# Kernel tuning notes

Measured on AMD Instinct MI355X. Metric: run time of the kernel, lower is better.

## Reference

```python
import jax, jax.numpy as jnp
import numpy as np

B = 1048576  # batch size
D = 16       # in_dim == hid_dim == out_dim (required by the torch matmul broadcasting)


def setup_inputs() -> dict:
    key = jax.random.key(0)
    kx, kw = jax.random.split(key)
    x = jax.random.normal(kx, (B, D), dtype=jnp.float32)
    W = jax.random.normal(kw, (D, D, D), dtype=jnp.float32) * (1.0 / D)
    return {"x": x, "W": W}


def reference(x, W):
    # Original torch: xBx = x @ W @ x.T permuted, then take the batch diagonal.
    # Mathematically: out[b, k] = sum_{i, j} x[b, i] * W[k, i, j] * x[b, j]
    # (batched bilinear/quadratic form per output channel k). We compute only
    # the needed diagonal terms instead of the full BxB cross-batch product.
    return jnp.einsum('bi,kij,bj->bk', x, W, x)
```

## Files before the change

### kernel.cpp

```cpp
#include <hip/hip_runtime.h>
#include <hip/hip_bf16.h>


typedef __attribute__((ext_vector_type(8)))  short  short8;
typedef __attribute__((ext_vector_type(8)))  __bf16 bf16x8;
typedef __attribute__((ext_vector_type(4)))  float  floatx4;

#define DEV static __device__ __forceinline__

constexpr int  alpha_of(int c) { return (c < 32) ? (c & 3) : (c - 32); }
constexpr int  beta_of(int c)  { return (c < 32) ? ((c & 3) + (c >> 2)) : (c - 32 + 8); }
constexpr bool live_of(int c)  { return c < 36; }

template <int C>
DEV float pval(const float* xv) {
    if constexpr (!live_of(C)) return 0.f;
    else return xv[alpha_of(C)] * xv[beta_of(C)];
}

template <int S>
DEV short8 make_afrag(const float* xv) {
    union { short8 s; __hip_bfloat162 h[4]; } u;
    u.h[0] = __float22bfloat162_rn(make_float2(pval<8 * S + 0>(xv), pval<8 * S + 1>(xv)));
    u.h[1] = __float22bfloat162_rn(make_float2(pval<8 * S + 2>(xv), pval<8 * S + 3>(xv)));
    u.h[2] = __float22bfloat162_rn(make_float2(pval<8 * S + 4>(xv), pval<8 * S + 5>(xv)));
    u.h[3] = __float22bfloat162_rn(make_float2(pval<8 * S + 6>(xv), pval<8 * S + 7>(xv)));
    return u.s;
}

DEV floatx4 mfma_bf16(short8 a, short8 b, floatx4 c) {
    return __builtin_amdgcn_mfma_f32_16x16x32_bf16(
        __builtin_bit_cast(bf16x8, a), __builtin_bit_cast(bf16x8, b), c, 0, 0, 0);
}

DEV float q_elem(const float* __restrict__ W, int e) {
    const int n = e / 160;
    const int k = e - n * 160;
    const int s = k >> 5, q = (k >> 3) & 3, j = k & 7;
    const int c = 8 * s + j;
    float qv = 0.f;
    if (c < 36) {
        const int a = (c < 32) ? (c & 3) : (c - 32);
        const int b = (c < 32) ? ((c & 3) + (c >> 2)) : (c - 32 + 8);
        const float w = (c < 32) ? 1.0f : 0.5f;
        const int I = (a + 4 * q) & 15, J = (b + 4 * q) & 15;
        qv = (I == J) ? W[n * 256 + I * 16 + I]
                      : w * (W[n * 256 + I * 16 + J] + W[n * 256 + J * 16 + I]);
    }
    return qv;
}

__global__ __launch_bounds__(256, 8)
void bilinear16_kernel(const float* __restrict__ x, const float* __restrict__ W,
                       float* __restrict__ out, int ntiles) {
    __shared__ __align__(16) short Qt[16][160];
    const int tid = threadIdx.x;
    for (int e = tid; e < 16 * 160; e += 256) {
        __hip_bfloat16 h = __float2bfloat16(q_elem(W, e));
        Qt[0][e] = *reinterpret_cast<short*>(&h);
    }
    __syncthreads();

    const int lane = tid & 63;
    const int n    = lane & 15;
    const int q    = lane >> 4;

    const short8 b0 = *reinterpret_cast<const short8*>(&Qt[n][0 * 32 + q * 8]);
    const short8 b1 = *reinterpret_cast<const short8*>(&Qt[n][1 * 32 + q * 8]);
    const short8 b2 = *reinterpret_cast<const short8*>(&Qt[n][2 * 32 + q * 8]);
    const short8 b3 = *reinterpret_cast<const short8*>(&Qt[n][3 * 32 + q * 8]);
    const short8 b4 = *reinterpret_cast<const short8*>(&Qt[n][4 * 32 + q * 8]);

    const int waveId = blockIdx.x * 4 + (tid >> 6);
    const int nwaves = gridDim.x * 4;

    for (int t = waveId; t < ntiles; t += nwaves) {
        const float4* xr = reinterpret_cast<const float4*>(x + (size_t)(t * 16 + n) * 16);
        const float4 c0 = xr[q];
        const float4 c1 = xr[(q + 1) & 3];
        const float4 c2 = xr[(q + 2) & 3];
        const float xv[12] = {c0.x, c0.y, c0.z, c0.w,
                              c1.x, c1.y, c1.z, c1.w,
                              c2.x, c2.y, c2.z, c2.w};

        floatx4 acc = {0.f, 0.f, 0.f, 0.f};
        acc = mfma_bf16(make_afrag<0>(xv), b0, acc);
        acc = mfma_bf16(make_afrag<1>(xv), b1, acc);
        acc = mfma_bf16(make_afrag<2>(xv), b2, acc);
        acc = mfma_bf16(make_afrag<3>(xv), b3, acc);
        acc = mfma_bf16(make_afrag<4>(xv), b4, acc);

        float* ob = out + (size_t)t * 256 + q * 64 + n;
        ob[0]  = acc[0];
        ob[16] = acc[1];
        ob[32] = acc[2];
        ob[48] = acc[3];
    }
}

extern "C" void kernel_launch(void* const* d_in, const int* in_sizes, int n_in,
                              void* d_out, int out_size, void* d_ws, size_t ws_size,
                              hipStream_t stream) {
    const float* x = (const float*)d_in[0];
    const float* W = (const float*)d_in[1];
    float* out = (float*)d_out;
    const int Bn = in_sizes[0] / 16;
    const int ntiles = Bn >> 4;
    bilinear16_kernel<<<2048, 256, 0, stream>>>(x, W, out, ntiles);
}
```

Before: 126.5 us.

## Load one float4 per lane with shuffles and stage outputs for coalesced stores

```diff
diff --git a/kernel.cpp b/kernel.cpp
--- a/kernel.cpp
+++ b/kernel.cpp
@@ -8,14 +8,29 @@
 
 #define DEV static __device__ __forceinline__
 
-constexpr int  alpha_of(int c) { return (c < 32) ? (c & 3) : (c - 32); }
-constexpr int  beta_of(int c)  { return (c < 32) ? ((c & 3) + (c >> 2)) : (c - 32 + 8); }
-constexpr bool live_of(int c)  { return c < 36; }
+constexpr int cA(int c) {
+    if (c < 24) { const int dIdx = c >> 1, v = c & 1;
+        const int hi = dIdx / 3, lo = dIdx % 3 + 1;
+        const int base = (hi == 3) ? 1 : 0;
+        const int l = v ? ((lo == 1) ? 2 : 1) : 0;
+        return base * 4 + l; }
+    if (c < 36) { const int g = c - 24, hi = g / 4 + 1, l = g & 3;
+        const int base = (hi == 3) ? 1 : 0;
+        return base * 4 + l; }
+    return c - 36;
+}
+constexpr int cDd(int c) {
+    if (c < 24) { const int dIdx = c >> 1;
+        return (dIdx / 3) * 4 + (dIdx % 3 + 1); }
+    if (c < 36) { return ((c - 24) / 4 + 1) * 4; }
+    return 0;
+}
+constexpr int   cB(int c) { return cA(c) ^ cDd(c); }
+constexpr float cW(int c) { return (c >= 24 && c < 36) ? 0.5f : 1.0f; }
 
 template <int C>
 DEV float pval(const float* xv) {
-    if constexpr (!live_of(C)) return 0.f;
-    else return xv[alpha_of(C)] * xv[beta_of(C)];
+    return xv[cA(C)] * xv[cB(C)];
 }
 
 template <int S>
@@ -38,22 +53,18 @@
     const int k = e - n * 160;
     const int s = k >> 5, q = (k >> 3) & 3, j = k & 7;
     const int c = 8 * s + j;
-    float qv = 0.f;
-    if (c < 36) {
-        const int a = (c < 32) ? (c & 3) : (c - 32);
-        const int b = (c < 32) ? ((c & 3) + (c >> 2)) : (c - 32 + 8);
-        const float w = (c < 32) ? 1.0f : 0.5f;
-        const int I = (a + 4 * q) & 15, J = (b + 4 * q) & 15;
-        qv = (I == J) ? W[n * 256 + I * 16 + I]
-                      : w * (W[n * 256 + I * 16 + J] + W[n * 256 + J * 16 + I]);
-    }
-    return qv;
+    const int I = cA(c) ^ (q << 2);
+    const int J = cB(c) ^ (q << 2);
+    return (I == J) ? W[n * 256 + I * 16 + I]
+                    : cW(c) * (W[n * 256 + I * 16 + J] + W[n * 256 + J * 16 + I]);
 }
 
 __global__ __launch_bounds__(256, 8)
 void bilinear16_kernel(const float* __restrict__ x, const float* __restrict__ W,
                        float* __restrict__ out, int ntiles) {
     __shared__ __align__(16) short Qt[16][160];
+    __shared__ __align__(16) float Tb[4][320];
+
     const int tid = threadIdx.x;
     for (int e = tid; e < 16 * 160; e += 256) {
         __hip_bfloat16 h = __float2bfloat16(q_elem(W, e));
@@ -64,6 +75,7 @@
     const int lane = tid & 63;
     const int n    = lane & 15;
     const int q    = lane >> 4;
+    float* const tb = Tb[tid >> 6];
 
     const short8 b0 = *reinterpret_cast<const short8*>(&Qt[n][0 * 32 + q * 8]);
     const short8 b1 = *reinterpret_cast<const short8*>(&Qt[n][1 * 32 + q * 8]);
@@ -75,13 +87,16 @@
     const int nwaves = gridDim.x * 4;
 
     for (int t = waveId; t < ntiles; t += nwaves) {
-        const float4* xr = reinterpret_cast<const float4*>(x + (size_t)(t * 16 + n) * 16);
-        const float4 c0 = xr[q];
-        const float4 c1 = xr[(q + 1) & 3];
-        const float4 c2 = xr[(q + 2) & 3];
-        const float xv[12] = {c0.x, c0.y, c0.z, c0.w,
-                              c1.x, c1.y, c1.z, c1.w,
-                              c2.x, c2.y, c2.z, c2.w};
+        const float4 own = *reinterpret_cast<const float4*>(
+            x + (size_t)t * 256 + n * 16 + q * 4);
+        float4 s1, s2;
+        s1.x = __shfl_xor(own.x, 16); s1.y = __shfl_xor(own.y, 16);
+        s1.z = __shfl_xor(own.z, 16); s1.w = __shfl_xor(own.w, 16);
+        s2.x = __shfl_xor(own.x, 32); s2.y = __shfl_xor(own.y, 32);
+        s2.z = __shfl_xor(own.z, 32); s2.w = __shfl_xor(own.w, 32);
+        const float xv[12] = {own.x, own.y, own.z, own.w,
+                              s1.x,  s1.y,  s1.z,  s1.w,
+                              s2.x,  s2.y,  s2.z,  s2.w};
 
         floatx4 acc = {0.f, 0.f, 0.f, 0.f};
         acc = mfma_bf16(make_afrag<0>(xv), b0, acc);
@@ -90,11 +105,13 @@
         acc = mfma_bf16(make_afrag<3>(xv), b3, acc);
         acc = mfma_bf16(make_afrag<4>(xv), b4, acc);
 
-        float* ob = out + (size_t)t * 256 + q * 64 + n;
-        ob[0]  = acc[0];
-        ob[16] = acc[1];
-        ob[32] = acc[2];
-        ob[48] = acc[3];
+        tb[(q * 4 + 0) * 20 + n] = acc[0];
+        tb[(q * 4 + 1) * 20 + n] = acc[1];
+        tb[(q * 4 + 2) * 20 + n] = acc[2];
+        tb[(q * 4 + 3) * 20 + n] = acc[3];
+        const float4 o = *reinterpret_cast<const float4*>(
+            &tb[(lane >> 2) * 20 + (lane & 3) * 4]);
+        *reinterpret_cast<float4*>(out + (size_t)t * 256 + lane * 4) = o;
     }
 }
 
```

New measurement: 122.6 us. 3.0% less time.
